# Kernel tuning notes

Measured on AMD Instinct MI355X. Metric: run time of the kernel, lower is better.

Reference implementation:

```python
import jax, jax.numpy as jnp
import numpy as np

DIM = 1024
MAXLEN = 2048
EPS = 1e-6


def rms_norm(x, w):
    rms = jnp.sqrt(jnp.mean(x * x, axis=-1, keepdims=True) + EPS)
    return x / rms * w


def setup_inputs() -> dict:
    key = jax.random.key(0)
    ks = jax.random.split(key, 12)
    d = DIM
    s = 0.02
    inp = {
        "x": jax.random.normal(ks[0], (8, 2048, d), dtype=jnp.float32),
        "attn_norm_w": jnp.ones((d,), jnp.float32),
        "mlp_norm_w": jnp.ones((d,), jnp.float32),
        "wq": jax.random.normal(ks[1], (d, d), jnp.float32) * s,
        "bq": jnp.zeros((d,), jnp.float32),
        "wk": jax.random.normal(ks[2], (d, d), jnp.float32) * s,
        "bk": jnp.zeros((d,), jnp.float32),
        "wv": jax.random.normal(ks[3], (d, d), jnp.float32) * s,
        "bv": jnp.zeros((d,), jnp.float32),
        "wo": jax.random.normal(ks[4], (d, d), jnp.float32) * s,
        "bo": jnp.zeros((d,), jnp.float32),
        "w1": jax.random.normal(ks[5], (d, 4 * d), jnp.float32) * s,
        "b1": jnp.zeros((4 * d,), jnp.float32),
        "w2": jax.random.normal(ks[6], (4 * d, d), jnp.float32) * s,
        "b2": jnp.zeros((d,), jnp.float32),
    }
    return inp


def reference(x, attn_norm_w, mlp_norm_w, wq, bq, wk, bk, wv, bv, wo, bo, w1, b1, w2, b2):
    b, t, d = x.shape
    xn = rms_norm(x, attn_norm_w)
    q = xn @ wq + bq
    k = xn @ wk + bk
    v = xn @ wv + bv
    # single-head attention over full dim, scaled by sqrt(d)
    scores = jnp.einsum("btd,bsd->bts", q, k) / jnp.sqrt(jnp.asarray(d, x.dtype))
    causal = jnp.tril(jnp.ones((t, t), dtype=bool))
    scores = jnp.where(causal, scores, jnp.asarray(-1e9, x.dtype))
    probs = jax.nn.softmax(scores, axis=-1)
    attn = jnp.einsum("bts,bsd->btd", probs, v)
    x = x + attn @ wo + bo
    h = rms_norm(x, mlp_norm_w)
    x = x + jax.nn.gelu(h @ w1 + b1, approximate=False) @ w2 + b2
    return x
```

## Files before the change

### kernel.cpp

```cpp
#include <hip/hip_runtime.h>
#include <hip/hip_bf16.h>

typedef __bf16 bf16;
typedef __bf16 bf16x8 __attribute__((ext_vector_type(8)));
typedef __bf16 bf16x4 __attribute__((ext_vector_type(4)));
typedef float  f32x4  __attribute__((ext_vector_type(4)));

#define DIM   1024
#define SEQ   2048
#define BATCH 8
#define NROWS (BATCH * SEQ)
#define HID   4096

__device__ __forceinline__ void async_ld16(const bf16* g, bf16* l) {
    __builtin_amdgcn_global_load_lds(
        (__attribute__((address_space(1))) void*)(g),
        (__attribute__((address_space(3))) void*)(l),
        16, 0, 0);
}

__device__ __forceinline__ f32x4 mfma16(bf16x8 a, bf16x8 b, f32x4 c) {
    return __builtin_amdgcn_mfma_f32_16x16x32_bf16(a, b, c, 0, 0, 0);
}

template<int OUTF32, int BIASMODE, int RESID, int GELU, int SCORE, int PV>
__global__ __launch_bounds__(512, 2) void gemm256_kernel(
    const bf16* __restrict__ A, size_t aB,
    const bf16* __restrict__ B, size_t bB,
    void* __restrict__ Cv, size_t cB,
    const float* __restrict__ bias,
    const float* __restrict__ resid,
    int M, int N, int K, float scale)
{
    __shared__ alignas(16) bf16 LA[2 * 2 * 8192];
    __shared__ alignas(16) bf16 LB[2 * 2 * 8192];

    const int gx = gridDim.x;
    int lin = blockIdx.y * gx + blockIdx.x;
    {
        const int nwg = gx * gridDim.y;
        const int q = nwg >> 3, r = nwg & 7;
        const int xcd = lin & 7, o = lin >> 3;
        lin = (xcd < r ? xcd * (q + 1) : r * (q + 1) + (xcd - r) * q) + o;
    }
    const int m0 = (lin / gx) * 256;
    const int n0 = (lin % gx) * 256;
    if (SCORE && n0 >= m0 + 256) return;

    const int z = blockIdx.z;
    A += (size_t)z * aB;
    B += (size_t)z * bB;

    const int t    = threadIdx.x;
    const int lane = t & 63;
    const int wave = t >> 6;
    const int wm   = wave >> 2;
    const int wn   = wave & 3;

    const int kEnd = PV ? (m0 + 256) : K;
    const int NT   = kEnd >> 6;

    const int srow = t >> 3;
    const int sd   = ((t & 7) ^ (srow & 7)) * 8;
    const bf16* gA = A + (size_t)(m0 + srow) * (size_t)K + sd;
    const bf16* gB = B + (size_t)(n0 + srow) * (size_t)K + sd;
    bf16* const lA = LA + wave * 512;
    bf16* const lB = LB + wave * 512;
    const size_t rowblk = (size_t)64 * (size_t)K;

#define STG_A(db, hf, T) do {                                               \
    const bf16* g_ = gA + (size_t)((hf) * 2) * rowblk + (size_t)(T) * 64;   \
    async_ld16(g_,          lA + ((db) * 2 + (hf)) * 8192);                 \
    async_ld16(g_ + rowblk, lA + ((db) * 2 + (hf)) * 8192 + 4096);          \
} while (0)
#define STG_B(db, hf, T) do {                                               \
    const bf16* g_ = gB + (size_t)((hf) * 2) * rowblk + (size_t)(T) * 64;   \
    async_ld16(g_,          lB + ((db) * 2 + (hf)) * 8192);                 \
    async_ld16(g_ + rowblk, lB + ((db) * 2 + (hf)) * 8192 + 4096);          \
} while (0)

    const int fr    = lane & 15;
    const int fg    = lane >> 4;
    const int pc0   = ((fg)     ^ (fr & 7)) * 8;
    const int pc1   = ((4 + fg) ^ (fr & 7)) * 8;
    const int raOff = wm * 8192 + fr * 64;
    const int rbOff = (wn >> 1) * 8192 + ((wn & 1) * 64 + fr) * 64;

    f32x4  acc[2][2][4][2] = {};
    bf16x8 af[4][2];
    bf16x8 bg[2][2][2];

#define LDF_A(db, qm) do { _Pragma("unroll")                                  \
    for (int mi_ = 0; mi_ < 4; ++mi_) {                                       \
        const bf16* p_ = LA + (db) * 16384 + raOff + ((qm) * 64 + mi_ * 16) * 64; \
        af[mi_][0] = *(const bf16x8*)(p_ + pc0);                              \
        af[mi_][1] = *(const bf16x8*)(p_ + pc1); } } while (0)
#define LDF_B(db, qn) do { _Pragma("unroll")                                  \
    for (int ni_ = 0; ni_ < 2; ++ni_) {                                       \
        const bf16* p_ = LB + (db) * 16384 + rbOff + ((qn) * 32 + ni_ * 16) * 64; \
        bg[qn][ni_][0] = *(const bf16x8*)(p_ + pc0);                          \
        bg[qn][ni_][1] = *(const bf16x8*)(p_ + pc1); } } while (0)
#define MFMAQ(qm, qn) do {                                                    \
    __builtin_amdgcn_s_setprio(1);                                            \
    _Pragma("unroll") for (int mi_ = 0; mi_ < 4; ++mi_)                       \
    _Pragma("unroll") for (int ni_ = 0; ni_ < 2; ++ni_) {                     \
        acc[qm][qn][mi_][ni_] = mfma16(af[mi_][0], bg[qn][ni_][0], acc[qm][qn][mi_][ni_]); \
        acc[qm][qn][mi_][ni_] = mfma16(af[mi_][1], bg[qn][ni_][1], acc[qm][qn][mi_][ni_]); } \
    __builtin_amdgcn_s_setprio(0);                                            \
} while (0)
#define LGKM0 do { asm volatile("s_waitcnt lgkmcnt(0)" ::: "memory");         \
                   __builtin_amdgcn_sched_barrier(0); } while (0)
#define LGKH  asm volatile("s_waitcnt lgkmcnt(8)" ::: "memory")
#define VM4   asm volatile("s_waitcnt vmcnt(4)" ::: "memory")
#define BAR   __builtin_amdgcn_s_barrier()

    STG_A(0, 0, 0); STG_A(0, 1, 0); STG_B(0, 0, 0); STG_B(0, 1, 0);
    STG_B(1, 0, 1); STG_B(1, 1, 1);
    VM4;
    BAR;

    for (int kt = 0; kt < NT; kt += 2) {
        const int Tp2 = (kt + 2 < NT) ? kt + 2 : NT - 1;
        const int Tp3 = (kt + 3 < NT) ? kt + 3 : NT - 1;

        LDF_A(0, 0); LDF_B(0, 0);
        STG_A(1, 0, kt + 1); STG_A(1, 1, kt + 1);
        LGKH; BAR; LGKM0; MFMAQ(0, 0); BAR;
        LDF_B(0, 1);
        BAR; LGKM0; MFMAQ(0, 1); BAR;
        LDF_A(0, 1);
        STG_B(0, 0, Tp2);
        BAR; LGKM0; MFMAQ(1, 0); BAR;
        STG_B(0, 1, Tp2);
        BAR; LGKM0; MFMAQ(1, 1); VM4; BAR;

        LDF_A(1, 0); LDF_B(1, 0);
        STG_A(0, 0, Tp2); STG_A(0, 1, Tp2);
        LGKH; BAR; LGKM0; MFMAQ(0, 0); BAR;
        LDF_B(1, 1);
        BAR; LGKM0; MFMAQ(0, 1); BAR;
        LDF_A(1, 1);
        STG_B(1, 0, Tp3);
        BAR; LGKM0; MFMAQ(1, 0); BAR;
        STG_B(1, 1, Tp3);
        BAR; LGKM0; MFMAQ(1, 1); VM4; BAR;
    }

    const int col  = lane & 15;
    const int row4 = (lane >> 4) * 4;
    const size_t cOff = (size_t)z * cB;
    #pragma unroll
    for (int qm = 0; qm < 2; ++qm)
    #pragma unroll
    for (int mi = 0; mi < 4; ++mi) {
        const int mBase = m0 + wm * 128 + qm * 64 + mi * 16 + row4;
        #pragma unroll
        for (int qn = 0; qn < 2; ++qn)
        #pragma unroll
        for (int ni = 0; ni < 2; ++ni) {
            const int n = n0 + wn * 64 + qn * 32 + ni * 16 + col;
            const float bcol = (BIASMODE == 1) ? bias[n] : 0.0f;
            #pragma unroll
            for (int r = 0; r < 4; ++r) {
                const int m = mBase + r;
                float v = acc[qm][qn][mi][ni][r];
                if (BIASMODE == 1) v += bcol;
                if (BIASMODE == 2) v += bias[m];
                if (SCORE) { v *= scale; if (n > m) v = -1e30f; }
                if (GELU)  { v = 0.5f * v * (1.0f + erff(v * 0.70710678118654752f)); }
                const size_t idx = cOff + (size_t)m * (size_t)N + (size_t)n;
                if (RESID) v += resid[idx];
                if (OUTF32) ((float*)Cv)[idx] = v;
                else        ((bf16*)Cv)[idx]  = (bf16)v;
            }
        }
    }
#undef STG_A
#undef STG_B
#undef LDF_A
#undef LDF_B
#undef MFMAQ
#undef LGKM0
#undef LGKH
#undef VM4
#undef BAR
}

__global__ __launch_bounds__(256) void rmsnorm_kernel(
    const float* __restrict__ x, const float* __restrict__ w, bf16* __restrict__ out)
{
    const int row = blockIdx.x;
    const int t   = threadIdx.x;
    const float4 v = ((const float4*)(x + (size_t)row * DIM))[t];
    float ss = v.x * v.x + v.y * v.y + v.z * v.z + v.w * v.w;
    #pragma unroll
    for (int off = 32; off; off >>= 1) ss += __shfl_down(ss, off);
    __shared__ float part[4];
    if ((t & 63) == 0) part[t >> 6] = ss;
    __syncthreads();
    const float tot  = part[0] + part[1] + part[2] + part[3];
    const float rinv = rsqrtf(tot * (1.0f / DIM) + 1e-6f);
    const float4 wv = ((const float4*)w)[t];
    bf16x4 o;
    o[0] = (bf16)(v.x * rinv * wv.x);
    o[1] = (bf16)(v.y * rinv * wv.y);
    o[2] = (bf16)(v.z * rinv * wv.z);
    o[3] = (bf16)(v.w * rinv * wv.w);
    *(bf16x4*)(out + (size_t)row * DIM + t * 4) = o;
}

__global__ __launch_bounds__(256) void transpose_w_kernel(
    const float* __restrict__ src, bf16* __restrict__ dst, int R, int C)
{
    __shared__ float tile[32][33];
    const int tx = threadIdx.x & 31;
    const int ty = threadIdx.x >> 5;
    const int c0 = blockIdx.x * 32;
    const int r0 = blockIdx.y * 32;
    #pragma unroll
    for (int j = 0; j < 32; j += 8)
        tile[ty + j][tx] = src[(size_t)(r0 + ty + j) * C + c0 + tx];
    __syncthreads();
    #pragma unroll
    for (int j = 0; j < 32; j += 8)
        dst[(size_t)(c0 + ty + j) * R + r0 + tx] = (bf16)tile[tx][ty + j];
}

__global__ __launch_bounds__(256) void softmax_kernel(bf16* __restrict__ S)
{
    const int t = blockIdx.x;
    const int b = blockIdx.y;
    bf16* p = S + ((size_t)b * SEQ + t) * SEQ;
    const int send = ((t >> 8) + 1) << 8;
    const int tid  = threadIdx.x;
    const int lane = tid & 63;
    const int wave = tid >> 6;

    float v[8];
    int cnt = 0;
    float m = -3.0e38f;
    for (int i = tid; i < send; i += 256) { const float f = (float)p[i]; v[cnt++] = f; m = fmaxf(m, f); }
    #pragma unroll
    for (int off = 32; off; off >>= 1) m = fmaxf(m, __shfl_down(m, off));
    __shared__ float red[4];
    if (lane == 0) red[wave] = m;
    __syncthreads();
    m = fmaxf(fmaxf(red[0], red[1]), fmaxf(red[2], red[3]));
    __syncthreads();

    float s = 0.0f;
    for (int k2 = 0; k2 < cnt; ++k2) { v[k2] = __expf(v[k2] - m); s += v[k2]; }
    #pragma unroll
    for (int off = 32; off; off >>= 1) s += __shfl_down(s, off);
    if (lane == 0) red[wave] = s;
    __syncthreads();
    s = red[0] + red[1] + red[2] + red[3];
    const float inv = 1.0f / s;
    cnt = 0;
    for (int i = tid; i < send; i += 256) p[i] = (bf16)(v[cnt++] * inv);
}

extern "C" void kernel_launch(void* const* d_in, const int* in_sizes, int n_in,
                              void* d_out, int out_size, void* d_ws, size_t ws_size,
                              hipStream_t stream)
{
    const float* x   = (const float*)d_in[0];
    const float* anw = (const float*)d_in[1];
    const float* mnw = (const float*)d_in[2];
    const float* wq  = (const float*)d_in[3];
    const float* bq  = (const float*)d_in[4];
    const float* wk  = (const float*)d_in[5];
    const float* bk  = (const float*)d_in[6];
    const float* wv  = (const float*)d_in[7];
    const float* bv  = (const float*)d_in[8];
    const float* wo  = (const float*)d_in[9];
    const float* bo  = (const float*)d_in[10];
    const float* w1  = (const float*)d_in[11];
    const float* b1  = (const float*)d_in[12];
    const float* w2  = (const float*)d_in[13];
    const float* b2  = (const float*)d_in[14];
    float* out = (float*)d_out;

    char* ws = (char*)d_ws;
    const size_t MB = 1024 * 1024;
    bf16* wqT = (bf16*)(ws + 0 * MB);
    bf16* wkT = (bf16*)(ws + 2 * MB);
    bf16* wvT = (bf16*)(ws + 4 * MB);
    bf16* woT = (bf16*)(ws + 6 * MB);
    bf16* w1T = (bf16*)(ws + 8 * MB);
    bf16* w2T = (bf16*)(ws + 16 * MB);
    bf16* xn  = (bf16*)(ws + 24 * MB);
    bf16* q   = (bf16*)(ws + 56 * MB);
    bf16* k   = (bf16*)(ws + 88 * MB);
    bf16* vT  = (bf16*)(ws + 120 * MB);
    bf16* S   = (bf16*)(ws + 152 * MB);
    bf16* attn = xn;
    bf16* h    = q;
    bf16* mid  = k;

    const dim3 blk(256);
    const dim3 blkG(512);

    transpose_w_kernel<<<dim3(DIM / 32, DIM / 32), blk, 0, stream>>>(wq, wqT, DIM, DIM);
    transpose_w_kernel<<<dim3(DIM / 32, DIM / 32), blk, 0, stream>>>(wk, wkT, DIM, DIM);
    transpose_w_kernel<<<dim3(DIM / 32, DIM / 32), blk, 0, stream>>>(wv, wvT, DIM, DIM);
    transpose_w_kernel<<<dim3(DIM / 32, DIM / 32), blk, 0, stream>>>(wo, woT, DIM, DIM);
    transpose_w_kernel<<<dim3(HID / 32, DIM / 32), blk, 0, stream>>>(w1, w1T, DIM, HID);
    transpose_w_kernel<<<dim3(DIM / 32, HID / 32), blk, 0, stream>>>(w2, w2T, HID, DIM);

    rmsnorm_kernel<<<NROWS, blk, 0, stream>>>(x, anw, xn);

    gemm256_kernel<0, 1, 0, 0, 0, 0><<<dim3(DIM / 256, NROWS / 256, 1), blkG, 0, stream>>>(
        xn, 0, wqT, 0, q, 0, bq, nullptr, NROWS, DIM, DIM, 1.0f);
    gemm256_kernel<0, 1, 0, 0, 0, 0><<<dim3(DIM / 256, NROWS / 256, 1), blkG, 0, stream>>>(
        xn, 0, wkT, 0, k, 0, bk, nullptr, NROWS, DIM, DIM, 1.0f);
    gemm256_kernel<0, 2, 0, 0, 0, 0><<<dim3(SEQ / 256, DIM / 256, BATCH), blkG, 0, stream>>>(
        wvT, 0, xn, (size_t)SEQ * DIM, vT, (size_t)DIM * SEQ, bv, nullptr, DIM, SEQ, DIM, 1.0f);

    gemm256_kernel<0, 0, 0, 0, 1, 0><<<dim3(SEQ / 256, SEQ / 256, BATCH), blkG, 0, stream>>>(
        q, (size_t)SEQ * DIM, k, (size_t)SEQ * DIM, S, (size_t)SEQ * SEQ,
        nullptr, nullptr, SEQ, SEQ, DIM, 0.03125f);

    softmax_kernel<<<dim3(SEQ, BATCH), blk, 0, stream>>>(S);

    gemm256_kernel<0, 0, 0, 0, 0, 1><<<dim3(DIM / 256, SEQ / 256, BATCH), blkG, 0, stream>>>(
        S, (size_t)SEQ * SEQ, vT, (size_t)DIM * SEQ, attn, (size_t)SEQ * DIM,
        nullptr, nullptr, SEQ, DIM, SEQ, 1.0f);

    gemm256_kernel<1, 1, 1, 0, 0, 0><<<dim3(DIM / 256, NROWS / 256, 1), blkG, 0, stream>>>(
        attn, 0, woT, 0, out, 0, bo, x, NROWS, DIM, DIM, 1.0f);

    rmsnorm_kernel<<<NROWS, blk, 0, stream>>>(out, mnw, h);

    gemm256_kernel<0, 1, 0, 1, 0, 0><<<dim3(HID / 256, NROWS / 256, 1), blkG, 0, stream>>>(
        h, 0, w1T, 0, mid, 0, b1, nullptr, NROWS, HID, DIM, 1.0f);

    gemm256_kernel<1, 1, 1, 0, 0, 0><<<dim3(DIM / 256, NROWS / 256, 1), blkG, 0, stream>>>(
        mid, 0, w2T, 0, out, 0, b2, out, NROWS, DIM, HID, 1.0f);
}
```

Before: 876.1 us.

## Simplify GEMM main loop to one barrier per k-tile with double buffering

```diff
diff --git a/kernel.cpp b/kernel.cpp
--- a/kernel.cpp
+++ b/kernel.cpp
@@ -101,49 +101,33 @@
         bg[qn][ni_][0] = *(const bf16x8*)(p_ + pc0);                          \
         bg[qn][ni_][1] = *(const bf16x8*)(p_ + pc1); } } while (0)
 #define MFMAQ(qm, qn) do {                                                    \
-    __builtin_amdgcn_s_setprio(1);                                            \
     _Pragma("unroll") for (int mi_ = 0; mi_ < 4; ++mi_)                       \
     _Pragma("unroll") for (int ni_ = 0; ni_ < 2; ++ni_) {                     \
         acc[qm][qn][mi_][ni_] = mfma16(af[mi_][0], bg[qn][ni_][0], acc[qm][qn][mi_][ni_]); \
         acc[qm][qn][mi_][ni_] = mfma16(af[mi_][1], bg[qn][ni_][1], acc[qm][qn][mi_][ni_]); } \
-    __builtin_amdgcn_s_setprio(0);                                            \
 } while (0)
-#define LGKM0 do { asm volatile("s_waitcnt lgkmcnt(0)" ::: "memory");         \
-                   __builtin_amdgcn_sched_barrier(0); } while (0)
-#define LGKH  asm volatile("s_waitcnt lgkmcnt(8)" ::: "memory")
-#define VM4   asm volatile("s_waitcnt vmcnt(4)" ::: "memory")
+#define VM0   asm volatile("s_waitcnt vmcnt(0)" ::: "memory")
 #define BAR   __builtin_amdgcn_s_barrier()
-
-    STG_A(0, 0, 0); STG_A(0, 1, 0); STG_B(0, 0, 0); STG_B(0, 1, 0);
-    STG_B(1, 0, 1); STG_B(1, 1, 1);
-    VM4;
-    BAR;
+#define PRIO1 __builtin_amdgcn_s_setprio(1)
+#define PRIO0 __builtin_amdgcn_s_setprio(0)
+
+#define KTILE(bufc, bufo, Tnx) do {                                           \
+    VM0; BAR;                                                                 \
+    STG_B(bufo, 0, Tnx); STG_B(bufo, 1, Tnx);                                 \
+    LDF_B(bufc, 0); LDF_B(bufc, 1); LDF_A(bufc, 0);                           \
+    PRIO1; MFMAQ(0, 0); MFMAQ(0, 1); PRIO0;                                   \
+    STG_A(bufo, 0, Tnx); STG_A(bufo, 1, Tnx);                                 \
+    LDF_A(bufc, 1);                                                           \
+    PRIO1; MFMAQ(1, 0); MFMAQ(1, 1); PRIO0;                                   \
+} while (0)
+
+    STG_B(0, 0, 0); STG_B(0, 1, 0); STG_A(0, 0, 0); STG_A(0, 1, 0);
 
     for (int kt = 0; kt < NT; kt += 2) {
+        const int Tp1 = kt + 1;
         const int Tp2 = (kt + 2 < NT) ? kt + 2 : NT - 1;
-        const int Tp3 = (kt + 3 < NT) ? kt + 3 : NT - 1;
-
-        LDF_A(0, 0); LDF_B(0, 0);
-        STG_A(1, 0, kt + 1); STG_A(1, 1, kt + 1);
-        LGKH; BAR; LGKM0; MFMAQ(0, 0); BAR;
-        LDF_B(0, 1);
-        BAR; LGKM0; MFMAQ(0, 1); BAR;
-        LDF_A(0, 1);
-        STG_B(0, 0, Tp2);
-        BAR; LGKM0; MFMAQ(1, 0); BAR;
-        STG_B(0, 1, Tp2);
-        BAR; LGKM0; MFMAQ(1, 1); VM4; BAR;
-
-        LDF_A(1, 0); LDF_B(1, 0);
-        STG_A(0, 0, Tp2); STG_A(0, 1, Tp2);
-        LGKH; BAR; LGKM0; MFMAQ(0, 0); BAR;
-        LDF_B(1, 1);
-        BAR; LGKM0; MFMAQ(0, 1); BAR;
-        LDF_A(1, 1);
-        STG_B(1, 0, Tp3);
-        BAR; LGKM0; MFMAQ(1, 0); BAR;
-        STG_B(1, 1, Tp3);
-        BAR; LGKM0; MFMAQ(1, 1); VM4; BAR;
+        KTILE(0, 1, Tp1);
+        KTILE(1, 0, Tp2);
     }
 
     const int col  = lane & 15;
@@ -180,10 +164,11 @@
 #undef LDF_A
 #undef LDF_B
 #undef MFMAQ
-#undef LGKM0
-#undef LGKH
-#undef VM4
+#undef VM0
 #undef BAR
+#undef PRIO1
+#undef PRIO0
+#undef KTILE
 }
 
 __global__ __launch_bounds__(256) void rmsnorm_kernel(
```

After: 946.2 us. 8.0% more time.
